# Performance work log

Measured on AMD Instinct MI355X. Metric: run time of the kernel, lower is better.

## Reference

```python
import jax, jax.numpy as jnp
import numpy as np

H, DH, CHUNK = 8, 64, 64      # heads, dim_head, chunk_size
DIM = 512
INNER = H * DH                # 512
EPS = 1e-5
SCALE = DH ** -0.5


def _ln(x, g, b):
    m = jnp.mean(x, -1, keepdims=True)
    v = jnp.mean((x - m) ** 2, -1, keepdims=True)
    return (x - m) * jax.lax.rsqrt(v + EPS) * g + b


def _heads(t):
    b, n, _ = t.shape
    return t.reshape(b, n, H, DH).transpose(0, 2, 1, 3)  # b h n d


def _merge(t):
    b, h, n, d = t.shape
    return t.transpose(0, 2, 1, 3).reshape(b, n, h * d)  # b n (h d)


def _local_attn(x, W_qkv, W_ao, b_ao):
    # PreNorm inner Attention: non-overlapping chunked local self-attention
    qkv = x @ W_qkv
    q, k, v = (jnp.split(qkv, 3, axis=-1))
    q, k, v = _heads(q), _heads(k), _heads(v)
    B, Hh, N, D = q.shape
    M = N // CHUNK
    qc = q.reshape(B, Hh, M, CHUNK, D)
    kc = k.reshape(B, Hh, M, CHUNK, D)
    vc = v.reshape(B, Hh, M, CHUNK, D)
    s = jnp.einsum('bhmcd,bhmkd->bhmck', qc, kc) * SCALE
    a = jax.nn.softmax(s, axis=-1)
    o = jnp.einsum('bhmck,bhmkd->bhmcd', a, vc).reshape(B, Hh, N, D)
    return _merge(o) @ W_ao + b_ao


def setup_inputs() -> dict:
    key = jax.random.key(0)
    ks = jax.random.split(key, 10)
    p = lambda k, shp: jax.random.normal(k, shp, dtype=jnp.float32) * 0.02
    return {
        'x':     jax.random.normal(ks[0], (2, 4096, DIM), dtype=jnp.float32),
        'q_x':   jax.random.normal(ks[1], (2, 2048, DIM), dtype=jnp.float32),
        'ln1_g': jnp.ones((DIM,), jnp.float32),
        'ln1_b': jnp.zeros((DIM,), jnp.float32),
        'W_qkv': p(ks[2], (DIM, INNER * 3)),
        'W_ao':  p(ks[3], (INNER, DIM)),
        'b_ao':  jnp.zeros((DIM,), jnp.float32),
        'ln2_g': jnp.ones((DIM,), jnp.float32),
        'ln2_b': jnp.zeros((DIM,), jnp.float32),
        'W_q':   p(ks[4], (DIM, INNER)),
        'W_kv':  p(ks[5], (DIM, INNER * 2)),
        'W_o':   p(ks[6], (INNER, DIM)),
        'b_o':   jnp.zeros((DIM,), jnp.float32),
    }


def reference(x, q_x, ln1_g, ln1_b, W_qkv, W_ao, b_ao,
              ln2_g, ln2_b, W_q, W_kv, W_o, b_o):
    # inner chunked self-attn with PreNorm + residual
    q_in = _local_attn(_ln(q_x, ln1_g, ln1_b), W_qkv, W_ao, b_ao) + q_x
    q_in = _ln(q_in, ln2_g, ln2_b)
    # full cross-attention: queries from q_in, keys/values from x
    q = _heads(q_in @ W_q)
    k, v = jnp.split(x @ W_kv, 2, axis=-1)
    k, v = _heads(k), _heads(v)
    s = jnp.einsum('bhqd,bhkd->bhqk', q, k) * SCALE
    a = jax.nn.softmax(s, axis=-1)
    out = _merge(jnp.einsum('bhqk,bhkd->bhqd', a, v)) @ W_o + b_o
    return (out, q_in)
```

## Files before the change

### kernel.cpp

```cpp
#include <hip/hip_runtime.h>

typedef unsigned short u16;
typedef unsigned int u32;
typedef __attribute__((ext_vector_type(4))) float f32x4;
typedef __attribute__((ext_vector_type(8))) __bf16 bf16x8;

#define NQ 2048
#define NK 4096
#define SCALE 0.125f
#define LOG2E 1.44269504088896f

__device__ __forceinline__ u16 f2bf(float f) {
  u32 x = __float_as_uint(f);
  return (u16)((x + 0x7fffu + ((x >> 16) & 1u)) >> 16);
}

__device__ __forceinline__ float bf2f(u16 b) {
  return __uint_as_float(((u32)b) << 16);
}

__device__ __forceinline__ int swz(int row, int colbyte) {
  return row * 128 + (colbyte ^ ((row & 7) << 4));
}

__device__ __forceinline__ void async16(u16* lds, const u16* g) {
  __builtin_amdgcn_global_load_lds(
      (const __attribute__((address_space(1))) void*)g,
      (__attribute__((address_space(3))) void*)lds, 16, 0, 0);
}

__device__ __forceinline__ f32x4 mfma16(bf16x8 a, bf16x8 b, f32x4 c) {
  return __builtin_amdgcn_mfma_f32_16x16x32_bf16(a, b, c, 0, 0, 0);
}

__device__ __forceinline__ float max16(const f32x4* s) {
  float a = fmaxf(fmaxf(s[0][0], s[0][1]), fmaxf(s[0][2], s[0][3]));
  float b = fmaxf(fmaxf(s[1][0], s[1][1]), fmaxf(s[1][2], s[1][3]));
  float c = fmaxf(fmaxf(s[2][0], s[2][1]), fmaxf(s[2][2], s[2][3]));
  float d = fmaxf(fmaxf(s[3][0], s[3][1]), fmaxf(s[3][2], s[3][3]));
  return fmaxf(fmaxf(a, b), fmaxf(c, d));
}

__global__ __launch_bounds__(256) void k_prep(
    const float* __restrict__ Wqkv, const float* __restrict__ Wao,
    const float* __restrict__ Wq, const float* __restrict__ Wkv,
    const float* __restrict__ Wo, const float* __restrict__ x,
    const float* __restrict__ qx, const float* __restrict__ ln1g,
    const float* __restrict__ ln1b,
    u16* __restrict__ o_qkv, u16* __restrict__ o_ao, u16* __restrict__ o_q,
    u16* __restrict__ o_kv, u16* __restrict__ o_o, u16* __restrict__ x_bf,
    u16* __restrict__ xn_bf) {
  int bid = blockIdx.x;
  int t = threadIdx.x;
  if (bid < 8192) {
    int idx = bid * 256 + t;
    int r = idx >> 9, k = idx & 511;
    const float* in;
    u16* out;
    int N, n;
    if (r < 1536)      { in = Wqkv; out = o_qkv; N = 1536; n = r; }
    else if (r < 2048) { in = Wao;  out = o_ao;  N = 512;  n = r - 1536; }
    else if (r < 2560) { in = Wq;   out = o_q;   N = 512;  n = r - 2048; }
    else if (r < 3584) { in = Wkv;  out = o_kv;  N = 1024; n = r - 2560; }
    else               { in = Wo;   out = o_o;   N = 512;  n = r - 3584; }
    out[(size_t)n * 512 + k] = f2bf(in[(size_t)k * N + n]);
  } else if (bid < 10240) {
    size_t i = ((size_t)(bid - 8192) * 256 + t) * 8;
    float v[8];
    *(float4*)&v[0] = *(const float4*)(x + i);
    *(float4*)&v[4] = *(const float4*)(x + i + 4);
    u16 o[8];
#pragma unroll
    for (int j = 0; j < 8; j++) o[j] = f2bf(v[j]);
    *(uint4*)(x_bf + i) = *(uint4*)o;
  } else {
    int row = (bid - 10240) * 4 + (t >> 6);
    int lane = t & 63;
    size_t base = (size_t)row * 512 + lane * 8;
    float v[8];
    *(float4*)&v[0] = *(const float4*)(qx + base);
    *(float4*)&v[4] = *(const float4*)(qx + base + 4);
    float s = 0.f, q = 0.f;
#pragma unroll
    for (int j = 0; j < 8; j++) { s += v[j]; q += v[j] * v[j]; }
#pragma unroll
    for (int d = 1; d < 64; d <<= 1) {
      s += __shfl_xor(s, d, 64);
      q += __shfl_xor(q, d, 64);
    }
    float mean = s * (1.f / 512.f);
    float var = q * (1.f / 512.f) - mean * mean;
    float rstd = rsqrtf(var + 1e-5f);
    float gv[8], bv[8];
    *(float4*)&gv[0] = *(const float4*)(ln1g + lane * 8);
    *(float4*)&gv[4] = *(const float4*)(ln1g + lane * 8 + 4);
    *(float4*)&bv[0] = *(const float4*)(ln1b + lane * 8);
    *(float4*)&bv[4] = *(const float4*)(ln1b + lane * 8 + 4);
    u16 ob[8];
#pragma unroll
    for (int j = 0; j < 8; j++)
      ob[j] = f2bf((v[j] - mean) * rstd * gv[j] + bv[j]);
    *(uint4*)(xn_bf + base) = *(uint4*)ob;
  }
}

__global__ __launch_bounds__(64) void k_ln(const float* __restrict__ xin,
                                           const float* __restrict__ res,
                                           const float* __restrict__ gg,
                                           const float* __restrict__ bb,
                                           float* __restrict__ fout,
                                           u16* __restrict__ bfout) {
  int row = blockIdx.x, t = threadIdx.x;
  size_t base = (size_t)row * 512 + t * 8;
  float v[8];
  *(float4*)&v[0] = *(const float4*)(xin + base);
  *(float4*)&v[4] = *(const float4*)(xin + base + 4);
  if (res) {
    float r2[8];
    *(float4*)&r2[0] = *(const float4*)(res + base);
    *(float4*)&r2[4] = *(const float4*)(res + base + 4);
#pragma unroll
    for (int j = 0; j < 8; j++) v[j] += r2[j];
  }
  float s = 0.f, q = 0.f;
#pragma unroll
  for (int j = 0; j < 8; j++) { s += v[j]; q += v[j] * v[j]; }
#pragma unroll
  for (int d = 1; d < 64; d <<= 1) {
    s += __shfl_xor(s, d, 64);
    q += __shfl_xor(q, d, 64);
  }
  float mean = s * (1.f / 512.f);
  float var = q * (1.f / 512.f) - mean * mean;
  float rstd = rsqrtf(var + 1e-5f);
  float gv[8], bv[8];
  *(float4*)&gv[0] = *(const float4*)(gg + t * 8);
  *(float4*)&gv[4] = *(const float4*)(gg + t * 8 + 4);
  *(float4*)&bv[0] = *(const float4*)(bb + t * 8);
  *(float4*)&bv[4] = *(const float4*)(bb + t * 8 + 4);
  float y[8];
  u16 ob[8];
#pragma unroll
  for (int j = 0; j < 8; j++) {
    y[j] = (v[j] - mean) * rstd * gv[j] + bv[j];
    ob[j] = f2bf(y[j]);
  }
  if (fout) {
    *(float4*)(fout + base) = *(float4*)&y[0];
    *(float4*)(fout + base + 4) = *(float4*)&y[4];
  }
  if (bfout) *(uint4*)(bfout + base) = *(uint4*)ob;
}

__global__ __launch_bounds__(256) void k_mm0(
    const u16* __restrict__ xb, const u16* __restrict__ wkv,
    const u16* __restrict__ xn, const u16* __restrict__ wqkv,
    u16* __restrict__ kpk, u16* __restrict__ vtp, u16* __restrict__ qkv) {
  __shared__ u16 As[8192];
  __shared__ u16 Bs[8192];
  const int tid = threadIdx.x;
  const int lane = tid & 63, wid = tid >> 6;
  const int lr = lane & 15, g = lane >> 4;
  const int wr = wid >> 1, wc = wid & 1;
  const int srow = wid * 8 + (lane >> 3);
  const int scol = ((lane & 7) ^ (lane >> 3)) << 3;
  u16* lA = As + wid * 512;
  u16* lB = Bs + wid * 512;
  const size_t rK = (size_t)32 * 512;
  int bid = blockIdx.x;
  if (bid < 512) {
    int bx = bid & 7, by = bid >> 3;
    const int rowBase = by * 128, colBase = bx * 128;
    f32x4 acc[4][4] = {};
    const u16* gA = xb + (size_t)(rowBase + srow) * 512 + scol;
    const u16* gB = wkv + (size_t)(colBase + srow) * 512 + scol;
    for (int k0 = 0; k0 < 512; k0 += 64) {
#pragma unroll
      for (int r = 0; r < 4; r++) async16(lA + r * 2048, gA + r * rK + k0);
#pragma unroll
      for (int r = 0; r < 4; r++) async16(lB + r * 2048, gB + r * rK + k0);
      __syncthreads();
#pragma unroll
      for (int kk = 0; kk < 2; kk++) {
        bf16x8 af[4], bw[4];
#pragma unroll
        for (int fm = 0; fm < 4; fm++) {
          int row = wr * 64 + fm * 16 + lr;
          af[fm] = *(const bf16x8*)((const char*)As + row * 128 +
                                    (((kk * 4 + g) ^ (row & 7)) << 4));
        }
#pragma unroll
        for (int fn = 0; fn < 4; fn++) {
          int row = wc * 64 + fn * 16 + lr;
          bw[fn] = *(const bf16x8*)((const char*)Bs + row * 128 +
                                    (((kk * 4 + g) ^ (row & 7)) << 4));
        }
#pragma unroll
        for (int fm = 0; fm < 4; fm++)
#pragma unroll
          for (int fn = 0; fn < 4; fn++)
            acc[fm][fn] = mfma16(af[fm], bw[fn], acc[fm][fn]);
      }
      __syncthreads();
    }
#pragma unroll
    for (int fm = 0; fm < 4; fm++) {
#pragma unroll
      for (int fn = 0; fn < 4; fn++) {
        int row = rowBase + wr * 64 + fm * 16 + g * 4;
        int col = colBase + wc * 64 + fn * 16 + lr;
        int b = row >> 12, n = row & 4095, kt = n >> 6, key0 = n & 63;
        int h = (col >> 6) & 7, d = col & 63;
        size_t tbase = ((size_t)(((b << 3) + h) << 6) + kt) * 4096;
        if (col < 512) {
          u16* kd = kpk + tbase + (size_t)key0 * 64 + d;
          kd[0] = f2bf(acc[fm][fn][0]);
          kd[64] = f2bf(acc[fm][fn][1]);
          kd[128] = f2bf(acc[fm][fn][2]);
          kd[192] = f2bf(acc[fm][fn][3]);
        } else {
          u16 p4[4] = {f2bf(acc[fm][fn][0]), f2bf(acc[fm][fn][1]),
                       f2bf(acc[fm][fn][2]), f2bf(acc[fm][fn][3])};
          *(uint2*)(vtp + tbase + (size_t)d * 64 + key0) = *(uint2*)p4;
        }
      }
    }
  } else {
    int j = bid - 512;
    int bx = j % 12, by = j / 12;
    const int rowBase = by * 64, colBase = bx * 128;
    f32x4 acc[2][4] = {};
    const u16* gA = xn + (size_t)(rowBase + srow) * 512 + scol;
    const u16* gB = wqkv + (size_t)(colBase + srow) * 512 + scol;
    for (int k0 = 0; k0 < 512; k0 += 64) {
#pragma unroll
      for (int r = 0; r < 2; r++) async16(lA + r * 2048, gA + r * rK + k0);
#pragma unroll
      for (int r = 0; r < 4; r++) async16(lB + r * 2048, gB + r * rK + k0);
      __syncthreads();
#pragma unroll
      for (int kk = 0; kk < 2; kk++) {
        bf16x8 af[2], bw[4];
#pragma unroll
        for (int fm = 0; fm < 2; fm++) {
          int row = wr * 32 + fm * 16 + lr;
          af[fm] = *(const bf16x8*)((const char*)As + row * 128 +
                                    (((kk * 4 + g) ^ (row & 7)) << 4));
        }
#pragma unroll
        for (int fn = 0; fn < 4; fn++) {
          int row = wc * 64 + fn * 16 + lr;
          bw[fn] = *(const bf16x8*)((const char*)Bs + row * 128 +
                                    (((kk * 4 + g) ^ (row & 7)) << 4));
        }
#pragma unroll
        for (int fm = 0; fm < 2; fm++)
#pragma unroll
          for (int fn = 0; fn < 4; fn++)
            acc[fm][fn] = mfma16(af[fm], bw[fn], acc[fm][fn]);
      }
      __syncthreads();
    }
#pragma unroll
    for (int fm = 0; fm < 2; fm++) {
#pragma unroll
      for (int fn = 0; fn < 4; fn++) {
        int row = rowBase + wr * 32 + fm * 16 + g * 4;
        int col = colBase + wc * 64 + fn * 16 + lr;
#pragma unroll
        for (int r = 0; r < 4; r++)
          qkv[(size_t)(row + r) * 1536 + col] = f2bf(acc[fm][fn][r]);
      }
    }
  }
}

template <bool BIAS, bool OBF16>
__global__ __launch_bounds__(256) void k_gemm2(const u16* __restrict__ A,
                                               const u16* __restrict__ Bt,
                                               const float* __restrict__ bias,
                                               void* __restrict__ C, int M, int N, int K) {
  __shared__ u16 As[4096];
  __shared__ u16 Bs[8192];
  const int tid = threadIdx.x;
  const int lane = tid & 63, wid = tid >> 6;
  const int lr = lane & 15, g = lane >> 4;
  const int wr = wid >> 1, wc = wid & 1;
  const int rowBase = blockIdx.y * 64, colBase = blockIdx.x * 128;
  f32x4 acc[2][4] = {};
  const int srow = wid * 8 + (lane >> 3);
  const int scol = ((lane & 7) ^ (lane >> 3)) << 3;
  const u16* gA = A + (size_t)(rowBase + srow) * K + scol;
  const u16* gB = Bt + (size_t)(colBase + srow) * K + scol;
  u16* lA = As + wid * 512;
  u16* lB = Bs + wid * 512;
  const size_t rK = (size_t)32 * K;
  for (int k0 = 0; k0 < K; k0 += 64) {
#pragma unroll
    for (int r = 0; r < 2; r++) async16(lA + r * 2048, gA + r * rK + k0);
#pragma unroll
    for (int r = 0; r < 4; r++) async16(lB + r * 2048, gB + r * rK + k0);
    __syncthreads();
#pragma unroll
    for (int kk = 0; kk < 2; kk++) {
      bf16x8 af[2], bw[4];
#pragma unroll
      for (int fm = 0; fm < 2; fm++) {
        int row = wr * 32 + fm * 16 + lr;
        af[fm] = *(const bf16x8*)((const char*)As + row * 128 +
                                  (((kk * 4 + g) ^ (row & 7)) << 4));
      }
#pragma unroll
      for (int fn = 0; fn < 4; fn++) {
        int row = wc * 64 + fn * 16 + lr;
        bw[fn] = *(const bf16x8*)((const char*)Bs + row * 128 +
                                  (((kk * 4 + g) ^ (row & 7)) << 4));
      }
#pragma unroll
      for (int fm = 0; fm < 2; fm++)
#pragma unroll
        for (int fn = 0; fn < 4; fn++)
          acc[fm][fn] = mfma16(af[fm], bw[fn], acc[fm][fn]);
    }
    __syncthreads();
  }
#pragma unroll
  for (int fm = 0; fm < 2; fm++) {
#pragma unroll
    for (int fn = 0; fn < 4; fn++) {
      int row = rowBase + wr * 32 + fm * 16 + g * 4;
      int col = colBase + wc * 64 + fn * 16 + lr;
      float bvv = BIAS ? bias[col] : 0.f;
#pragma unroll
      for (int r = 0; r < 4; r++) {
        float v = acc[fm][fn][r] + bvv;
        if (OBF16)
          ((u16*)C)[(size_t)(row + r) * N + col] = f2bf(v);
        else
          ((float*)C)[(size_t)(row + r) * N + col] = v;
      }
    }
  }
}

__global__ __launch_bounds__(256) void k_local(const u16* __restrict__ qkv,
                                               u16* __restrict__ oattn) {
  int bid = blockIdx.x;
  int m = bid & 31, h = (bid >> 5) & 7, b = bid >> 8;
  __shared__ u16 Qs[4096], Ks[4096], Vt[4096], Ps[4096];
  int t = threadIdx.x;
  {
    int i = t >> 2, c0 = (t & 3) * 16;
    const u16* base = qkv + (size_t)(b * NQ + m * 64 + i) * 1536 + c0;
    uint4 q0 = *(const uint4*)(base + h * 64);
    uint4 q1 = *(const uint4*)(base + h * 64 + 8);
    uint4 k0 = *(const uint4*)(base + 512 + h * 64);
    uint4 k1 = *(const uint4*)(base + 512 + h * 64 + 8);
    uint4 v0 = *(const uint4*)(base + 1024 + h * 64);
    uint4 v1 = *(const uint4*)(base + 1024 + h * 64 + 8);
    *(uint4*)((char*)Qs + swz(i, c0 * 2)) = q0;
    *(uint4*)((char*)Qs + swz(i, c0 * 2 + 16)) = q1;
    *(uint4*)((char*)Ks + swz(i, c0 * 2)) = k0;
    *(uint4*)((char*)Ks + swz(i, c0 * 2 + 16)) = k1;
    u16 vv[16];
    *(uint4*)&vv[0] = v0;
    *(uint4*)&vv[8] = v1;
#pragma unroll
    for (int j = 0; j < 16; j++) {
      int d = c0 + j;
      *(u16*)((char*)Vt + swz(d, i * 2)) = vv[j];
    }
  }
  __syncthreads();
  int lane = t & 63, w = t >> 6, lr = lane & 15, g = lane >> 4;
  bf16x8 aq[2];
#pragma unroll
  for (int kk = 0; kk < 2; kk++)
    aq[kk] = *(const bf16x8*)((const char*)Qs + swz(w * 16 + lr, kk * 64 + g * 16));
  f32x4 s[4] = {};
#pragma unroll
  for (int fn = 0; fn < 4; fn++)
#pragma unroll
    for (int kk = 0; kk < 2; kk++) {
      bf16x8 bk = *(const bf16x8*)((const char*)Ks + swz(fn * 16 + lr, kk * 64 + g * 16));
      s[fn] = mfma16(aq[kk], bk, s[fn]);
    }
  float mx[4], sm[4], p[4][4];
#pragma unroll
  for (int r = 0; r < 4; r++)
    mx[r] = fmaxf(fmaxf(s[0][r], s[1][r]), fmaxf(s[2][r], s[3][r]));
#pragma unroll
  for (int d = 1; d < 16; d <<= 1)
#pragma unroll
    for (int r = 0; r < 4; r++) mx[r] = fmaxf(mx[r], __shfl_xor(mx[r], d, 64));
#pragma unroll
  for (int r = 0; r < 4; r++) {
    float a = 0.f;
#pragma unroll
    for (int fn = 0; fn < 4; fn++) {
      p[fn][r] = exp2f((s[fn][r] - mx[r]) * (SCALE * LOG2E));
      a += p[fn][r];
    }
    sm[r] = a;
  }
#pragma unroll
  for (int d = 1; d < 16; d <<= 1)
#pragma unroll
    for (int r = 0; r < 4; r++) sm[r] += __shfl_xor(sm[r], d, 64);
  float rinv[4];
#pragma unroll
  for (int r = 0; r < 4; r++) rinv[r] = 1.f / sm[r];
#pragma unroll
  for (int fn = 0; fn < 4; fn++)
#pragma unroll
    for (int r = 0; r < 4; r++)
      *(u16*)((char*)Ps + swz(w * 16 + g * 4 + r, (fn * 16 + lr) * 2)) =
          f2bf(p[fn][r] * rinv[r]);
  bf16x8 ap[2];
#pragma unroll
  for (int kk = 0; kk < 2; kk++)
    ap[kk] = *(const bf16x8*)((const char*)Ps + swz(w * 16 + lr, kk * 64 + g * 16));
  f32x4 o[4] = {};
#pragma unroll
  for (int fn = 0; fn < 4; fn++)
#pragma unroll
    for (int kk = 0; kk < 2; kk++) {
      bf16x8 bv = *(const bf16x8*)((const char*)Vt + swz(fn * 16 + lr, kk * 64 + g * 16));
      o[fn] = mfma16(ap[kk], bv, o[fn]);
    }
#pragma unroll
  for (int fn = 0; fn < 4; fn++)
#pragma unroll
    for (int r = 0; r < 4; r++)
      oattn[(size_t)(b * NQ + m * 64 + w * 16 + g * 4 + r) * 512 + h * 64 + fn * 16 + lr] =
          f2bf(o[fn][r]);
}

__global__ __launch_bounds__(256, 4) void k_cross(const u16* __restrict__ q,
                                                  const u16* __restrict__ kpk,
                                                  const u16* __restrict__ vtp,
                                                  u16* __restrict__ opart,
                                                  float* __restrict__ ml) {
  int f = blockIdx.x + 16 * blockIdx.y + 256 * blockIdx.z;
  int xcd = f & 7, j = f >> 3;
  int c = xcd + 8 * (j >> 4);
  int qt = j & 15, bh = c & 15, split = c >> 4;
  int b = bh >> 3, h = bh & 7;
  int t = threadIdx.x, lane = t & 63, w = t >> 6, lr = lane & 15, g = lane >> 4;
  __shared__ u16 Ks[2][4096], Vs[2][4096], Ps[4096];
  u16* pw = Ps + w * 1024;
  const float cs = SCALE * LOG2E;

  bf16x8 ones;
#pragma unroll
  for (int i = 0; i < 8; i++) ones[i] = (__bf16)1.0f;

  int srow = w * 16 + (lane >> 3);
  int soff0 = srow * 64 + (((lane & 7) ^ (srow & 7)) << 3);
  int soff1 = soff0 + 512;
  const u16* ktiles = kpk + ((size_t)(bh * 64 + split * 16) * 4096);
  const u16* vtiles = vtp + ((size_t)(bh * 64 + split * 16) * 4096);

  const u16* qrowL = q + (size_t)(b * NQ + qt * 128 + w * 32 + lr) * 512 + h * 64;
  const u16* qrowH = qrowL + 16 * 512;
  bf16x8 aqL0 = *(const bf16x8*)(qrowL + g * 8);
  bf16x8 aqL1 = *(const bf16x8*)(qrowL + 32 + g * 8);
  bf16x8 aqH0 = *(const bf16x8*)(qrowH + g * 8);
  bf16x8 aqH1 = *(const bf16x8*)(qrowH + 32 + g * 8);

  f32x4 oL[4] = {}, oH[4] = {};
  f32x4 lsumL = {}, lsumH = {};
  float mL = -1e30f, mH = -1e30f;

  async16(&Ks[0][w * 1024], ktiles + soff0);
  async16(&Ks[0][w * 1024 + 512], ktiles + soff1);
  async16(&Vs[0][w * 1024], vtiles + soff0);
  async16(&Vs[0][w * 1024 + 512], vtiles + soff1);
  __syncthreads();

  int buf = 0;
  for (int kt = 0; kt < 16; kt++) {
    if (kt < 15) {
      const u16* kn = ktiles + (size_t)(kt + 1) * 4096;
      const u16* vn = vtiles + (size_t)(kt + 1) * 4096;
      async16(&Ks[buf ^ 1][w * 1024], kn + soff0);
      async16(&Ks[buf ^ 1][w * 1024 + 512], kn + soff1);
      async16(&Vs[buf ^ 1][w * 1024], vn + soff0);
      async16(&Vs[buf ^ 1][w * 1024 + 512], vn + soff1);
    }
    f32x4 stL[4], stH[4];
    __builtin_amdgcn_s_setprio(1);
#pragma unroll
    for (int fm = 0; fm < 4; fm++) {
      bf16x8 bk0 = *(const bf16x8*)((const char*)Ks[buf] + swz(fm * 16 + lr, g * 16));
      bf16x8 bk1 = *(const bf16x8*)((const char*)Ks[buf] + swz(fm * 16 + lr, 64 + g * 16));
      stL[fm] = mfma16(bk0, aqL0, (f32x4){0.f, 0.f, 0.f, 0.f});
      stL[fm] = mfma16(bk1, aqL1, stL[fm]);
      stH[fm] = mfma16(bk0, aqH0, (f32x4){0.f, 0.f, 0.f, 0.f});
      stH[fm] = mfma16(bk1, aqH1, stH[fm]);
    }
    __builtin_amdgcn_s_setprio(0);
    float tmL = max16(stL);
    tmL = fmaxf(tmL, __shfl_xor(tmL, 16, 64));
    tmL = fmaxf(tmL, __shfl_xor(tmL, 32, 64));
    if (!__all(tmL <= mL + 22.2f)) {
      float mnew = fmaxf(mL, tmL);
      float corr = exp2f((mL - mnew) * cs);
      mL = mnew;
      float c0 = __shfl(corr, g * 4 + 0, 64);
      float c1 = __shfl(corr, g * 4 + 1, 64);
      float c2 = __shfl(corr, g * 4 + 2, 64);
      float c3 = __shfl(corr, g * 4 + 3, 64);
      lsumL[0] *= c0; lsumL[1] *= c1; lsumL[2] *= c2; lsumL[3] *= c3;
#pragma unroll
      for (int fn = 0; fn < 4; fn++) {
        oL[fn][0] *= c0; oL[fn][1] *= c1; oL[fn][2] *= c2; oL[fn][3] *= c3;
      }
    }
    {
      float mc = mL * cs;
#pragma unroll
      for (int fm = 0; fm < 4; fm++) {
        float p0 = exp2f(stL[fm][0] * cs - mc);
        float p1 = exp2f(stL[fm][1] * cs - mc);
        float p2 = exp2f(stL[fm][2] * cs - mc);
        float p3 = exp2f(stL[fm][3] * cs - mc);
        union { __bf16 hh[4]; uint2 vv; } pu;
        pu.hh[0] = (__bf16)p0; pu.hh[1] = (__bf16)p1;
        pu.hh[2] = (__bf16)p2; pu.hh[3] = (__bf16)p3;
        *(uint2*)((char*)pw + swz(lr, fm * 32 + g * 8)) = pu.vv;
      }
    }
    bf16x8 apL0 = *(const bf16x8*)((const char*)pw + swz(lr, g * 16));
    bf16x8 apL1 = *(const bf16x8*)((const char*)pw + swz(lr, 64 + g * 16));
    float tmH = max16(stH);
    tmH = fmaxf(tmH, __shfl_xor(tmH, 16, 64));
    tmH = fmaxf(tmH, __shfl_xor(tmH, 32, 64));
    if (!__all(tmH <= mH + 22.2f)) {
      float mnew = fmaxf(mH, tmH);
      float corr = exp2f((mH - mnew) * cs);
      mH = mnew;
      float c0 = __shfl(corr, g * 4 + 0, 64);
      float c1 = __shfl(corr, g * 4 + 1, 64);
      float c2 = __shfl(corr, g * 4 + 2, 64);
      float c3 = __shfl(corr, g * 4 + 3, 64);
      lsumH[0] *= c0; lsumH[1] *= c1; lsumH[2] *= c2; lsumH[3] *= c3;
#pragma unroll
      for (int fn = 0; fn < 4; fn++) {
        oH[fn][0] *= c0; oH[fn][1] *= c1; oH[fn][2] *= c2; oH[fn][3] *= c3;
      }
    }
    {
      float mc = mH * cs;
#pragma unroll
      for (int fm = 0; fm < 4; fm++) {
        float p0 = exp2f(stH[fm][0] * cs - mc);
        float p1 = exp2f(stH[fm][1] * cs - mc);
        float p2 = exp2f(stH[fm][2] * cs - mc);
        float p3 = exp2f(stH[fm][3] * cs - mc);
        union { __bf16 hh[4]; uint2 vv; } pu;
        pu.hh[0] = (__bf16)p0; pu.hh[1] = (__bf16)p1;
        pu.hh[2] = (__bf16)p2; pu.hh[3] = (__bf16)p3;
        *(uint2*)((char*)pw + swz(lr, fm * 32 + g * 8)) = pu.vv;
      }
    }
    bf16x8 apH0 = *(const bf16x8*)((const char*)pw + swz(lr, g * 16));
    bf16x8 apH1 = *(const bf16x8*)((const char*)pw + swz(lr, 64 + g * 16));
    __builtin_amdgcn_s_setprio(1);
    lsumL = mfma16(apL0, ones, lsumL);
    lsumL = mfma16(apL1, ones, lsumL);
    lsumH = mfma16(apH0, ones, lsumH);
    lsumH = mfma16(apH1, ones, lsumH);
#pragma unroll
    for (int fn = 0; fn < 4; fn++) {
      bf16x8 bv0 = *(const bf16x8*)((const char*)Vs[buf] + swz(fn * 16 + lr, g * 16));
      bf16x8 bv1 = *(const bf16x8*)((const char*)Vs[buf] + swz(fn * 16 + lr, 64 + g * 16));
      oL[fn] = mfma16(apL0, bv0, oL[fn]);
      oL[fn] = mfma16(apL1, bv1, oL[fn]);
      oH[fn] = mfma16(apH0, bv0, oH[fn]);
      oH[fn] = mfma16(apH1, bv1, oH[fn]);
    }
    __builtin_amdgcn_s_setprio(0);
    __syncthreads();
    buf ^= 1;
  }
  size_t sb = ((size_t)(split * 16 + bh) * NQ) + qt * 128 + w * 32;
  {
    float r0 = 1.f / lsumL[0], r1 = 1.f / lsumL[1];
    float r2 = 1.f / lsumL[2], r3 = 1.f / lsumL[3];
#pragma unroll
    for (int fn = 0; fn < 4; fn++) {
      opart[(sb + g * 4 + 0) * 64 + fn * 16 + lr] = f2bf(oL[fn][0] * r0);
      opart[(sb + g * 4 + 1) * 64 + fn * 16 + lr] = f2bf(oL[fn][1] * r1);
      opart[(sb + g * 4 + 2) * 64 + fn * 16 + lr] = f2bf(oL[fn][2] * r2);
      opart[(sb + g * 4 + 3) * 64 + fn * 16 + lr] = f2bf(oL[fn][3] * r3);
    }
  }
  {
    float r0 = 1.f / lsumH[0], r1 = 1.f / lsumH[1];
    float r2 = 1.f / lsumH[2], r3 = 1.f / lsumH[3];
#pragma unroll
    for (int fn = 0; fn < 4; fn++) {
      opart[(sb + 16 + g * 4 + 0) * 64 + fn * 16 + lr] = f2bf(oH[fn][0] * r0);
      opart[(sb + 16 + g * 4 + 1) * 64 + fn * 16 + lr] = f2bf(oH[fn][1] * r1);
      opart[(sb + 16 + g * 4 + 2) * 64 + fn * 16 + lr] = f2bf(oH[fn][2] * r2);
      opart[(sb + 16 + g * 4 + 3) * 64 + fn * 16 + lr] = f2bf(oH[fn][3] * r3);
    }
  }
  if (g == 0) {
    ml[(sb + lr) * 2] = mL;
    ml[(sb + 16 + lr) * 2] = mH;
  }
  if (lr == 0) {
#pragma unroll
    for (int r = 0; r < 4; r++) {
      ml[(sb + g * 4 + r) * 2 + 1] = lsumL[r];
      ml[(sb + 16 + g * 4 + r) * 2 + 1] = lsumH[r];
    }
  }
}

__global__ __launch_bounds__(256) void k_comb(const u16* __restrict__ opart,
                                              const float* __restrict__ ml,
                                              u16* __restrict__ co) {
  int idx = blockIdx.x * 256 + threadIdx.x;
  int c8 = idx & 7;
  int row = (idx >> 3) & 2047;
  int bh = idx >> 14;
  int b = bh >> 3, h = bh & 7;
  const float cs = SCALE * LOG2E;
  float m[4], l[4];
#pragma unroll
  for (int s = 0; s < 4; s++) {
    size_t rb = ((size_t)(s * 16 + bh) * NQ + row);
    m[s] = ml[rb * 2];
    l[s] = ml[rb * 2 + 1];
  }
  float M = fmaxf(fmaxf(m[0], m[1]), fmaxf(m[2], m[3]));
  float wsum = 0.f, wgt[4];
#pragma unroll
  for (int s = 0; s < 4; s++) {
    wgt[s] = l[s] * exp2f((m[s] - M) * cs);
    wsum += wgt[s];
  }
  float acc[8] = {};
#pragma unroll
  for (int s = 0; s < 4; s++) {
    size_t rb = ((size_t)(s * 16 + bh) * NQ + row);
    uint4 pk = *(const uint4*)(opart + rb * 64 + c8 * 8);
    u16 pe[8];
    *(uint4*)pe = pk;
#pragma unroll
    for (int j = 0; j < 8; j++) acc[j] += wgt[s] * bf2f(pe[j]);
  }
  float rw = 1.f / wsum;
  u16 ob[8];
#pragma unroll
  for (int j = 0; j < 8; j++) ob[j] = f2bf(acc[j] * rw);
  *(uint4*)(co + ((size_t)(b * NQ + row) * 512) + h * 64 + c8 * 8) = *(uint4*)ob;
}

extern "C" void kernel_launch(void* const* d_in, const int* in_sizes, int n_in,
                              void* d_out, int out_size, void* d_ws, size_t ws_size,
                              hipStream_t stream) {
  const float* x    = (const float*)d_in[0];
  const float* qx   = (const float*)d_in[1];
  const float* ln1g = (const float*)d_in[2];
  const float* ln1b = (const float*)d_in[3];
  const float* Wqkv = (const float*)d_in[4];
  const float* Wao  = (const float*)d_in[5];
  const float* bao  = (const float*)d_in[6];
  const float* ln2g = (const float*)d_in[7];
  const float* ln2b = (const float*)d_in[8];
  const float* Wq   = (const float*)d_in[9];
  const float* Wkv  = (const float*)d_in[10];
  const float* Wo   = (const float*)d_in[11];
  const float* bo   = (const float*)d_in[12];
  float* out_p = (float*)d_out;
  float* qin_p = out_p + (size_t)2 * 2048 * 512;

  const size_t MiB = 1048576;
  char* ws = (char*)d_ws;
  u16* w_qkv_t = (u16*)(ws);
  u16* w_ao_t  = (u16*)(ws + 1572864);
  u16* w_q_t   = (u16*)(ws + 2097152);
  u16* w_kv_t  = (u16*)(ws + 2621440);
  u16* w_o_t   = (u16*)(ws + 3670016);
  u16* kpk     = (u16*)(ws + 4 * MiB);
  u16* vtp     = (u16*)(ws + 12 * MiB);
  u16* x_bf    = (u16*)(ws + 20 * MiB);
  u16* oattn_bf = (u16*)(ws + 20 * MiB);
  float* ao_f  = (float*)(ws + 24 * MiB);
  u16* xn_bf   = (u16*)(ws + 28 * MiB);
  u16* qin_bf  = (u16*)(ws + 32 * MiB);
  u16* opart   = (u16*)(ws + 20 * MiB);
  u16* qkv_bf  = (u16*)(ws + 36 * MiB);
  u16* q_bf    = (u16*)(ws + 36 * MiB);
  u16* co_bf   = (u16*)(ws + 40 * MiB);
  float* ml    = out_p;


  k_prep<<<dim3(8192 + 2048 + 1024), 256, 0, stream>>>(
      Wqkv, Wao, Wq, Wkv, Wo, x, qx, ln1g, ln1b,
      w_qkv_t, w_ao_t, w_q_t, w_kv_t, w_o_t, x_bf, xn_bf);
  k_mm0<<<dim3(512 + 768), 256, 0, stream>>>(
      x_bf, w_kv_t, xn_bf, w_qkv_t, kpk, vtp, qkv_bf);
  k_local<<<dim3(512), 256, 0, stream>>>(qkv_bf, oattn_bf);
  k_gemm2<true, false><<<dim3(512 / 128, 4096 / 64), 256, 0, stream>>>(
      oattn_bf, w_ao_t, bao, ao_f, 4096, 512, 512);
  k_ln<<<dim3(4096), 64, 0, stream>>>(ao_f, qx, ln2g, ln2b, qin_p, qin_bf);
  k_gemm2<false, true><<<dim3(512 / 128, 4096 / 64), 256, 0, stream>>>(
      qin_bf, w_q_t, nullptr, q_bf, 4096, 512, 512);
  k_cross<<<dim3(16, 16, 4), 256, 0, stream>>>(q_bf, kpk, vtp, opart, ml);
  k_comb<<<dim3(262144 / 256), 256, 0, stream>>>(opart, ml, co_bf);
  k_gemm2<true, false><<<dim3(512 / 128, 4096 / 64), 256, 0, stream>>>(
      co_bf, w_o_t, bo, out_p, 4096, 512, 512);
}
```

Measured before the change: 158.8 us.

## Keep softmax probabilities in registers via permuted K layout; shrink GEMM tiles

In the cross-attention kernel, the K tile is loaded into shared memory with a permuted row order. This makes each lane's score-MFMA output line up with the A-operand layout the PV MFMA needs, so the exponentiated probabilities are packed directly into registers. That removes the per-tile shared-memory round trip through the P buffer and frees its LDS. Separately, the projection GEMMs switch from 64x128 to 64x64 tiles, doubling the block count to 512 for better occupancy across CUs, at the cost of less B reuse per block.

```diff
diff --git a/kernel.cpp b/kernel.cpp
--- a/kernel.cpp
+++ b/kernel.cpp
@@ -276,18 +276,18 @@
 }
 
 template <bool BIAS, bool OBF16>
-__global__ __launch_bounds__(256) void k_gemm2(const u16* __restrict__ A,
+__global__ __launch_bounds__(256) void k_gemm3(const u16* __restrict__ A,
                                                const u16* __restrict__ Bt,
                                                const float* __restrict__ bias,
                                                void* __restrict__ C, int M, int N, int K) {
   __shared__ u16 As[4096];
-  __shared__ u16 Bs[8192];
+  __shared__ u16 Bs[4096];
   const int tid = threadIdx.x;
   const int lane = tid & 63, wid = tid >> 6;
   const int lr = lane & 15, g = lane >> 4;
   const int wr = wid >> 1, wc = wid & 1;
-  const int rowBase = blockIdx.y * 64, colBase = blockIdx.x * 128;
-  f32x4 acc[2][4] = {};
+  const int rowBase = blockIdx.y * 64, colBase = blockIdx.x * 64;
+  f32x4 acc[2][2] = {};
   const int srow = wid * 8 + (lane >> 3);
   const int scol = ((lane & 7) ^ (lane >> 3)) << 3;
   const u16* gA = A + (size_t)(rowBase + srow) * K + scol;
@@ -299,11 +299,11 @@
 #pragma unroll
     for (int r = 0; r < 2; r++) async16(lA + r * 2048, gA + r * rK + k0);
 #pragma unroll
-    for (int r = 0; r < 4; r++) async16(lB + r * 2048, gB + r * rK + k0);
+    for (int r = 0; r < 2; r++) async16(lB + r * 2048, gB + r * rK + k0);
     __syncthreads();
 #pragma unroll
     for (int kk = 0; kk < 2; kk++) {
-      bf16x8 af[2], bw[4];
+      bf16x8 af[2], bw[2];
 #pragma unroll
       for (int fm = 0; fm < 2; fm++) {
         int row = wr * 32 + fm * 16 + lr;
@@ -311,15 +311,15 @@
                                   (((kk * 4 + g) ^ (row & 7)) << 4));
       }
 #pragma unroll
-      for (int fn = 0; fn < 4; fn++) {
-        int row = wc * 64 + fn * 16 + lr;
+      for (int fn = 0; fn < 2; fn++) {
+        int row = wc * 32 + fn * 16 + lr;
         bw[fn] = *(const bf16x8*)((const char*)Bs + row * 128 +
                                   (((kk * 4 + g) ^ (row & 7)) << 4));
       }
 #pragma unroll
       for (int fm = 0; fm < 2; fm++)
 #pragma unroll
-        for (int fn = 0; fn < 4; fn++)
+        for (int fn = 0; fn < 2; fn++)
           acc[fm][fn] = mfma16(af[fm], bw[fn], acc[fm][fn]);
     }
     __syncthreads();
@@ -327,9 +327,9 @@
 #pragma unroll
   for (int fm = 0; fm < 2; fm++) {
 #pragma unroll
-    for (int fn = 0; fn < 4; fn++) {
+    for (int fn = 0; fn < 2; fn++) {
       int row = rowBase + wr * 32 + fm * 16 + g * 4;
-      int col = colBase + wc * 64 + fn * 16 + lr;
+      int col = colBase + wc * 32 + fn * 16 + lr;
       float bvv = BIAS ? bias[col] : 0.f;
 #pragma unroll
       for (int r = 0; r < 4; r++) {
@@ -447,8 +447,7 @@
   int qt = j & 15, bh = c & 15, split = c >> 4;
   int b = bh >> 3, h = bh & 7;
   int t = threadIdx.x, lane = t & 63, w = t >> 6, lr = lane & 15, g = lane >> 4;
-  __shared__ u16 Ks[2][4096], Vs[2][4096], Ps[4096];
-  u16* pw = Ps + w * 1024;
+  __shared__ u16 Ks[2][4096], Vs[2][4096];
   const float cs = SCALE * LOG2E;
 
   bf16x8 ones;
@@ -456,7 +455,12 @@
   for (int i = 0; i < 8; i++) ones[i] = (__bf16)1.0f;
 
   int srow = w * 16 + (lane >> 3);
-  int soff0 = srow * 64 + (((lane & 7) ^ (srow & 7)) << 3);
+  int scolb = ((lane & 7) ^ (srow & 7)) << 3;
+  int kperm = ((srow >> 5) << 5) + (((srow >> 2) & 3) << 3) +
+              (((srow >> 4) & 1) << 2) + (srow & 3);
+  int ksoff0 = kperm * 64 + scolb;
+  int ksoff1 = ksoff0 + 1024;
+  int soff0 = srow * 64 + scolb;
   int soff1 = soff0 + 512;
   const u16* ktiles = kpk + ((size_t)(bh * 64 + split * 16) * 4096);
   const u16* vtiles = vtp + ((size_t)(bh * 64 + split * 16) * 4096);
@@ -472,8 +476,8 @@
   f32x4 lsumL = {}, lsumH = {};
   float mL = -1e30f, mH = -1e30f;
 
-  async16(&Ks[0][w * 1024], ktiles + soff0);
-  async16(&Ks[0][w * 1024 + 512], ktiles + soff1);
+  async16(&Ks[0][w * 1024], ktiles + ksoff0);
+  async16(&Ks[0][w * 1024 + 512], ktiles + ksoff1);
   async16(&Vs[0][w * 1024], vtiles + soff0);
   async16(&Vs[0][w * 1024 + 512], vtiles + soff1);
   __syncthreads();
@@ -483,8 +487,8 @@
     if (kt < 15) {
       const u16* kn = ktiles + (size_t)(kt + 1) * 4096;
       const u16* vn = vtiles + (size_t)(kt + 1) * 4096;
-      async16(&Ks[buf ^ 1][w * 1024], kn + soff0);
-      async16(&Ks[buf ^ 1][w * 1024 + 512], kn + soff1);
+      async16(&Ks[buf ^ 1][w * 1024], kn + ksoff0);
+      async16(&Ks[buf ^ 1][w * 1024 + 512], kn + ksoff1);
       async16(&Vs[buf ^ 1][w * 1024], vn + soff0);
       async16(&Vs[buf ^ 1][w * 1024 + 512], vn + soff1);
     }
@@ -517,22 +521,20 @@
         oL[fn][0] *= c0; oL[fn][1] *= c1; oL[fn][2] *= c2; oL[fn][3] *= c3;
       }
     }
+    bf16x8 apL0, apL1;
     {
       float mc = mL * cs;
-#pragma unroll
-      for (int fm = 0; fm < 4; fm++) {
-        float p0 = exp2f(stL[fm][0] * cs - mc);
-        float p1 = exp2f(stL[fm][1] * cs - mc);
-        float p2 = exp2f(stL[fm][2] * cs - mc);
-        float p3 = exp2f(stL[fm][3] * cs - mc);
-        union { __bf16 hh[4]; uint2 vv; } pu;
-        pu.hh[0] = (__bf16)p0; pu.hh[1] = (__bf16)p1;
-        pu.hh[2] = (__bf16)p2; pu.hh[3] = (__bf16)p3;
-        *(uint2*)((char*)pw + swz(lr, fm * 32 + g * 8)) = pu.vv;
-      }
-    }
-    bf16x8 apL0 = *(const bf16x8*)((const char*)pw + swz(lr, g * 16));
-    bf16x8 apL1 = *(const bf16x8*)((const char*)pw + swz(lr, 64 + g * 16));
+      union { __bf16 hh[8]; bf16x8 v; } u0, u1;
+#pragma unroll
+      for (int r = 0; r < 4; r++) {
+        u0.hh[r]     = (__bf16)exp2f(stL[0][r] * cs - mc);
+        u0.hh[4 + r] = (__bf16)exp2f(stL[1][r] * cs - mc);
+        u1.hh[r]     = (__bf16)exp2f(stL[2][r] * cs - mc);
+        u1.hh[4 + r] = (__bf16)exp2f(stL[3][r] * cs - mc);
+      }
+      apL0 = u0.v;
+      apL1 = u1.v;
+    }
     float tmH = max16(stH);
     tmH = fmaxf(tmH, __shfl_xor(tmH, 16, 64));
     tmH = fmaxf(tmH, __shfl_xor(tmH, 32, 64));
@@ -550,22 +552,20 @@
         oH[fn][0] *= c0; oH[fn][1] *= c1; oH[fn][2] *= c2; oH[fn][3] *= c3;
       }
     }
+    bf16x8 apH0, apH1;
     {
       float mc = mH * cs;
-#pragma unroll
-      for (int fm = 0; fm < 4; fm++) {
-        float p0 = exp2f(stH[fm][0] * cs - mc);
-        float p1 = exp2f(stH[fm][1] * cs - mc);
-        float p2 = exp2f(stH[fm][2] * cs - mc);
-        float p3 = exp2f(stH[fm][3] * cs - mc);
-        union { __bf16 hh[4]; uint2 vv; } pu;
-        pu.hh[0] = (__bf16)p0; pu.hh[1] = (__bf16)p1;
-        pu.hh[2] = (__bf16)p2; pu.hh[3] = (__bf16)p3;
-        *(uint2*)((char*)pw + swz(lr, fm * 32 + g * 8)) = pu.vv;
-      }
-    }
-    bf16x8 apH0 = *(const bf16x8*)((const char*)pw + swz(lr, g * 16));
-    bf16x8 apH1 = *(const bf16x8*)((const char*)pw + swz(lr, 64 + g * 16));
+      union { __bf16 hh[8]; bf16x8 v; } u0, u1;
+#pragma unroll
+      for (int r = 0; r < 4; r++) {
+        u0.hh[r]     = (__bf16)exp2f(stH[0][r] * cs - mc);
+        u0.hh[4 + r] = (__bf16)exp2f(stH[1][r] * cs - mc);
+        u1.hh[r]     = (__bf16)exp2f(stH[2][r] * cs - mc);
+        u1.hh[4 + r] = (__bf16)exp2f(stH[3][r] * cs - mc);
+      }
+      apH0 = u0.v;
+      apH1 = u1.v;
+    }
     __builtin_amdgcn_s_setprio(1);
     lsumL = mfma16(apL0, ones, lsumL);
     lsumL = mfma16(apL1, ones, lsumL);
@@ -699,20 +699,19 @@
   u16* co_bf   = (u16*)(ws + 40 * MiB);
   float* ml    = out_p;
 
-
   k_prep<<<dim3(8192 + 2048 + 1024), 256, 0, stream>>>(
       Wqkv, Wao, Wq, Wkv, Wo, x, qx, ln1g, ln1b,
       w_qkv_t, w_ao_t, w_q_t, w_kv_t, w_o_t, x_bf, xn_bf);
   k_mm0<<<dim3(512 + 768), 256, 0, stream>>>(
       x_bf, w_kv_t, xn_bf, w_qkv_t, kpk, vtp, qkv_bf);
   k_local<<<dim3(512), 256, 0, stream>>>(qkv_bf, oattn_bf);
-  k_gemm2<true, false><<<dim3(512 / 128, 4096 / 64), 256, 0, stream>>>(
+  k_gemm3<true, false><<<dim3(512 / 64, 4096 / 64), 256, 0, stream>>>(
       oattn_bf, w_ao_t, bao, ao_f, 4096, 512, 512);
   k_ln<<<dim3(4096), 64, 0, stream>>>(ao_f, qx, ln2g, ln2b, qin_p, qin_bf);
-  k_gemm2<false, true><<<dim3(512 / 128, 4096 / 64), 256, 0, stream>>>(
+  k_gemm3<false, true><<<dim3(512 / 64, 4096 / 64), 256, 0, stream>>>(
       qin_bf, w_q_t, nullptr, q_bf, 4096, 512, 512);
   k_cross<<<dim3(16, 16, 4), 256, 0, stream>>>(q_bf, kpk, vtp, opart, ml);
   k_comb<<<dim3(262144 / 256), 256, 0, stream>>>(opart, ml, co_bf);
-  k_gemm2<true, false><<<dim3(512 / 128, 4096 / 64), 256, 0, stream>>>(
+  k_gemm3<true, false><<<dim3(512 / 64, 4096 / 64), 256, 0, stream>>>(
       co_bf, w_o_t, bo, out_p, 4096, 512, 512);
 }
```

Result: faster. 153.8 us (-3.1%).
